# Performance work log

Hardware: AMD Instinct MI355X
Metric: run time of the kernel (lower is better)

Reference implementation:

```python
import jax, jax.numpy as jnp
import numpy as np

EMBED_DIM = 1024
NUM_HEADS = 16
HEAD_DIM = EMBED_DIM // NUM_HEADS
SEQ_LEN = 2048
B = 2


def setup_inputs() -> dict:
    key = jax.random.key(0)
    ks = jax.random.split(key, 6)
    x = jax.random.normal(ks[0], (B, SEQ_LEN, EMBED_DIM), dtype=jnp.float32)
    # Linear params (torch Linear: y = x @ W.T + b); store W as [in, out] for einsum
    qkv_w = jax.random.normal(ks[1], (EMBED_DIM, 3 * EMBED_DIM), dtype=jnp.float32) * (EMBED_DIM ** -0.5)
    qkv_b = jnp.zeros((3 * EMBED_DIM,), dtype=jnp.float32)
    proj_w = jax.random.normal(ks[2], (EMBED_DIM, EMBED_DIM), dtype=jnp.float32) * (EMBED_DIM ** -0.5)
    proj_b = jnp.zeros((EMBED_DIM,), dtype=jnp.float32)
    # relative position bias table [2L-1, H], trunc_normal std=0.02 ~ normal*0.02
    bias_table = jax.random.normal(ks[3], (2 * SEQ_LEN - 1, NUM_HEADS), dtype=jnp.float32) * 0.02
    return {"x": x, "qkv_w": qkv_w, "qkv_b": qkv_b, "proj_w": proj_w, "proj_b": proj_b, "bias_table": bias_table}


def _rel_pos_index(L):
    coords = jnp.arange(L)
    return (coords[None, :] - coords[:, None]) + (SEQ_LEN - 1)  # [L, L] int


def reference(x, qkv_w, qkv_b, proj_w, proj_b, bias_table):
    Bsz, L, C = x.shape
    scale = HEAD_DIM ** -0.5
    qkv = x @ qkv_w + qkv_b                               # [B, L, 3C]
    qkv = qkv.reshape(Bsz, L, 3, NUM_HEADS, HEAD_DIM)
    q = jnp.transpose(qkv[:, :, 0], (0, 2, 1, 3))          # [B, H, L, D]
    k = jnp.transpose(qkv[:, :, 1], (0, 2, 1, 3))
    v = jnp.transpose(qkv[:, :, 2], (0, 2, 1, 3))
    attn = jnp.einsum('bhqd,bhkd->bhqk', q, k) * scale     # [B, H, L, L]
    rel_bias = bias_table[_rel_pos_index(L)]               # [L, L, H]
    attn = attn + jnp.transpose(rel_bias, (2, 0, 1))[None]  # broadcast over batch
    attn = jax.nn.softmax(attn, axis=-1)
    out = jnp.einsum('bhqk,bhkd->bhqd', attn, v)           # [B, H, L, D]
    out = jnp.transpose(out, (0, 2, 1, 3)).reshape(Bsz, L, C)
    return out @ proj_w + proj_b
```

## Files before the change

### kernel.cpp

```cpp
#include <hip/hip_runtime.h>

typedef short bf16x4 __attribute__((ext_vector_type(4)));
typedef short bf16x8 __attribute__((ext_vector_type(8)));
typedef float f32x4 __attribute__((ext_vector_type(4)));
typedef float f32x16 __attribute__((ext_vector_type(16)));

__device__ __forceinline__ unsigned short f2bf(float f) {
  union { float f; unsigned int u; } v; v.f = f;
  unsigned int r = v.u + 0x7FFFu + ((v.u >> 16) & 1u);
  return (unsigned short)(r >> 16);
}

__device__ __forceinline__ float exp2_fast(float x) {
  float r;
  asm("v_exp_f32 %0, %1" : "=v"(r) : "v"(x));
  return r;
}

__device__ __forceinline__ unsigned int cvt_pk_bf16(float lo, float hi) {
  unsigned int r;
  asm("v_cvt_pk_bf16_f32 %0, %1, %2" : "=v"(r) : "v"(lo), "v"(hi));
  return r;
}

__device__ __forceinline__ void gld_lds16(const void* g, void* l) {
  __builtin_amdgcn_global_load_lds(
      (const __attribute__((address_space(1))) unsigned int*)g,
      (__attribute__((address_space(3))) unsigned int*)l, 16, 0, 0);
}


__global__ __launch_bounds__(256) void k_convert_x(const float4* __restrict__ in,
                                                   ushort4* __restrict__ out) {
  int id = blockIdx.x * 256 + threadIdx.x;
  float4 v = in[id];
  ushort4 o;
  o.x = f2bf(v.x); o.y = f2bf(v.y); o.z = f2bf(v.z); o.w = f2bf(v.w);
  out[id] = o;
}

__global__ __launch_bounds__(256) void k_transpose_bf16(const float* __restrict__ in,
                                                        unsigned short* __restrict__ out,
                                                        int R, int C) {
  __shared__ float tile[32][33];
  int tx = threadIdx.x, ty = threadIdx.y;
  int c0 = blockIdx.x * 32, r0 = blockIdx.y * 32;
#pragma unroll
  for (int i = 0; i < 32; i += 8) tile[ty + i][tx] = in[(size_t)(r0 + ty + i) * C + c0 + tx];
  __syncthreads();
#pragma unroll
  for (int i = 0; i < 32; i += 8) out[(size_t)(c0 + ty + i) * R + r0 + tx] = f2bf(tile[tx][ty + i]);
}

__global__ __launch_bounds__(256) void k_bias_cols(const float* __restrict__ bt,
                                                   float* __restrict__ bh) {
  int i = blockIdx.x * 256 + threadIdx.x;
  if (i < 4095 * 16) bh[(i & 15) * 4096 + (i >> 4)] = bt[i] * 1.44269504089f;
}

template <int EPI>
__global__ __launch_bounds__(256) void k_gemm(const unsigned short* __restrict__ A,
                                              const unsigned short* __restrict__ Bt,
                                              const float* __restrict__ bias,
                                              float* __restrict__ Cf,
                                              unsigned short* __restrict__ qb,
                                              unsigned short* __restrict__ kb,
                                              unsigned short* __restrict__ vtb) {
  __shared__ unsigned short Alds[128 * 64];
  __shared__ unsigned short Blds[128 * 64];
  const int t = threadIdx.x;
  const int l = t & 63, w = t >> 6;
  const int l15 = l & 15, l4 = l >> 4;
  const int wm = w >> 1, wn = w & 1;
  const int bm = blockIdx.y * 128, bn = blockIdx.x * 128;

  const int srow = t >> 3;
  const int scl = (t & 7) ^ (srow & 7);
  const unsigned short* ag = A + (size_t)(bm + srow) * 1024 + scl * 8;
  const unsigned short* bg = Bt + (size_t)(bn + srow) * 1024 + scl * 8;

  f32x4 acc[4][4];
#pragma unroll
  for (int i = 0; i < 4; ++i)
#pragma unroll
    for (int j = 0; j < 4; ++j) acc[i][j] = (f32x4){0.f, 0.f, 0.f, 0.f};

  for (int kt = 0; kt < 16; ++kt) {
#pragma unroll
    for (int q = 0; q < 4; ++q) {
      gld_lds16(ag + (size_t)q * 32 * 1024 + kt * 64, &Alds[(q * 256 + t) * 8]);
      gld_lds16(bg + (size_t)q * 32 * 1024 + kt * 64, &Blds[(q * 256 + t) * 8]);
    }
    __syncthreads();
#pragma unroll
    for (int kc = 0; kc < 2; ++kc) {
      bf16x8 af[4], bv[4];
#pragma unroll
      for (int i = 0; i < 4; ++i) {
        int ra = wm * 64 + i * 16 + l15;
        af[i] = *(const bf16x8*)&Alds[ra * 64 + (((kc * 4 + l4) ^ (l15 & 7))) * 8];
        int rb = wn * 64 + i * 16 + l15;
        bv[i] = *(const bf16x8*)&Blds[rb * 64 + (((kc * 4 + l4) ^ (l15 & 7))) * 8];
      }
#pragma unroll
      for (int i = 0; i < 4; ++i)
#pragma unroll
        for (int jn = 0; jn < 4; ++jn)
          acc[i][jn] = __builtin_amdgcn_mfma_f32_16x16x32_bf16(af[i], bv[jn], acc[i][jn], 0, 0, 0);
    }
    __syncthreads();
  }

#pragma unroll
  for (int i = 0; i < 4; ++i) {
#pragma unroll
    for (int jn = 0; jn < 4; ++jn) {
      int n = bn + wn * 64 + jn * 16 + l15;
      float bval = bias[n];
#pragma unroll
      for (int j = 0; j < 4; ++j) {
        int m = bm + wm * 64 + i * 16 + l4 * 4 + j;
        float v = acc[i][jn][j] + bval;
        if (EPI == 0) {
          Cf[(size_t)m * 1024 + n] = v;
        } else {
          int which = n >> 10, hh = (n >> 6) & 15, d = n & 63;
          int bb = m >> 11, pos = m & 2047;
          int bhh = bb * 16 + hh;
          if (which == 0)
            qb[((size_t)bhh * 2048 + pos) * 64 + d] = f2bf(v * 0.18033688f);
          else if (which == 1)
            kb[((size_t)bhh * 2048 + pos) * 64 + d] = f2bf(v);
          else
            vtb[((size_t)bhh * 64 + d) * 2048 + pos] = f2bf(v);
        }
      }
    }
  }
}

__global__ __launch_bounds__(256) void k_attn(const unsigned short* __restrict__ qbuf,
                                              const unsigned short* __restrict__ kbuf,
                                              const unsigned short* __restrict__ vtbuf,
                                              const float* __restrict__ biash,
                                              unsigned short* __restrict__ aout) {
  __shared__ __align__(16) unsigned short Klds[2][64 * 64];
  __shared__ __align__(16) unsigned short Vlds[2][64 * 64];
  __shared__ __align__(16) float blds[4 * 2308];

  const int t = threadIdx.x;
  const int w = t >> 6, l = t & 63;
  const int l31 = l & 31, hi = l >> 5;
  const int bh = blockIdx.y;
  const int h = bh & 15, b = bh >> 4;
  const int qbase = blockIdx.x * 128;
  const int wq = qbase + w * 32;

  bf16x8 qB[4];
  {
    const unsigned short* qrow = qbuf + ((size_t)bh * 2048 + wq + l31) * 64;
#pragma unroll
    for (int ds = 0; ds < 4; ++ds) qB[ds] = *(const bf16x8*)&qrow[ds * 16 + hi * 8];
  }

  f32x16 O[2];
#pragma unroll
  for (int i = 0; i < 16; ++i) { O[0][i] = 0.f; O[1][i] = 0.f; }
  float m_run = -3e38f, l_run = 0.f;

  const int c0r = t >> 3, c0c = t & 7;
  const unsigned short* kg = kbuf + ((size_t)bh * 2048 + c0r) * 64 + c0c * 8;
  const unsigned short* vg = vtbuf + ((size_t)bh * 64 + c0r) * 2048 + c0c * 8;
  const int wKV = c0r * 64 + ((c0c ^ (c0r & 7)) * 8);

  {
    bf16x8 k0 = *(const bf16x8*)(kg);
    bf16x8 k1 = *(const bf16x8*)(kg + 32 * 64);
    bf16x8 v0 = *(const bf16x8*)(vg);
    bf16x8 v1 = *(const bf16x8*)(vg + 32 * 2048);
    *(bf16x8*)&Klds[0][wKV] = k0;
    *(bf16x8*)&Klds[0][wKV + 2048] = k1;
    *(bf16x8*)&Vlds[0][wKV] = v0;
    *(bf16x8*)&Vlds[0][wKV + 2048] = v1;
    const float* win = biash + h * 4096 + (1920 - qbase);
    for (int j = t; j < 2308; j += 256) {
#pragma unroll
      for (int c = 0; c < 4; ++c) {
        float v = (j + c <= 2174) ? win[j + c] : 0.f;
        blds[c * 2308 + j] = v;
      }
    }
  }
  __syncthreads();

  const int cb = (127 - l31) & 3;
  const float* bbase = blds + (cb * 2308 + 127 - l31 - 32 * w + 4 * hi - cb);

  for (int kt = 0; kt < 32; ++kt) {
    const int cur = kt & 1;

    bf16x8 kst0, kst1, vst0, vst1;
    if (kt < 31) {
      const unsigned short* kga = kg + (size_t)(kt + 1) * 4096;
      const unsigned short* vga = vg + (kt + 1) * 64;
      kst0 = *(const bf16x8*)(kga);
      kst1 = *(const bf16x8*)(kga + 32 * 64);
      vst0 = *(const bf16x8*)(vga);
      vst1 = *(const bf16x8*)(vga + 32 * 2048);
    }
    const int kbase = kt * 64;

    f32x16 sacc[2];
#pragma unroll
    for (int i = 0; i < 16; ++i) { sacc[0][i] = 0.f; sacc[1][i] = 0.f; }
    __builtin_amdgcn_s_setprio(1);
#pragma unroll
    for (int kt2 = 0; kt2 < 2; ++kt2) {
      int row = kt2 * 32 + l31;
      int rsw = row & 7;
#pragma unroll
      for (int ds = 0; ds < 4; ++ds) {
        bf16x8 ka = *(const bf16x8*)&Klds[cur][row * 64 + (((2 * ds + hi) ^ rsw) * 8)];
        sacc[kt2] = __builtin_amdgcn_mfma_f32_32x32x16_bf16(ka, qB[ds], sacc[kt2], 0, 0, 0);
      }
    }
    __builtin_amdgcn_s_setprio(0);

#pragma unroll
    for (int kt2 = 0; kt2 < 2; ++kt2)
#pragma unroll
      for (int g = 0; g < 4; ++g) {
        f32x4 bq = *(const f32x4*)&bbase[kbase + 32 * kt2 + 8 * g];
#pragma unroll
        for (int r = 0; r < 4; ++r) sacc[kt2][4 * g + r] += bq[r];
      }

    float mx;
    {
      float q0 = fmaxf(fmaxf(sacc[0][0], sacc[0][1]), fmaxf(sacc[0][2], sacc[0][3]));
      float q1 = fmaxf(fmaxf(sacc[0][4], sacc[0][5]), fmaxf(sacc[0][6], sacc[0][7]));
      float q2 = fmaxf(fmaxf(sacc[0][8], sacc[0][9]), fmaxf(sacc[0][10], sacc[0][11]));
      float q3 = fmaxf(fmaxf(sacc[0][12], sacc[0][13]), fmaxf(sacc[0][14], sacc[0][15]));
      float q4 = fmaxf(fmaxf(sacc[1][0], sacc[1][1]), fmaxf(sacc[1][2], sacc[1][3]));
      float q5 = fmaxf(fmaxf(sacc[1][4], sacc[1][5]), fmaxf(sacc[1][6], sacc[1][7]));
      float q6 = fmaxf(fmaxf(sacc[1][8], sacc[1][9]), fmaxf(sacc[1][10], sacc[1][11]));
      float q7 = fmaxf(fmaxf(sacc[1][12], sacc[1][13]), fmaxf(sacc[1][14], sacc[1][15]));
      mx = fmaxf(fmaxf(fmaxf(q0, q1), fmaxf(q2, q3)), fmaxf(fmaxf(q4, q5), fmaxf(q6, q7)));
      mx = fmaxf(mx, __shfl_xor(mx, 32));
    }

    if (__any(mx > m_run + 8.f)) {
      float mnew = fmaxf(m_run, mx);
      float alpha = exp2_fast(m_run - mnew);
      m_run = mnew;
      l_run *= alpha;
#pragma unroll
      for (int g = 0; g < 4; ++g)
#pragma unroll
        for (int r = 0; r < 4; ++r) {
          float a_lo = __shfl(alpha, 8 * g + r);
          float a_hi = __shfl(alpha, 8 * g + r + 4);
          float aq = hi ? a_hi : a_lo;
          O[0][4 * g + r] *= aq;
          O[1][4 * g + r] *= aq;
        }
    }

#pragma unroll
    for (int kt2 = 0; kt2 < 2; ++kt2)
#pragma unroll
      for (int i = 0; i < 16; ++i) sacc[kt2][i] = exp2_fast(sacc[kt2][i] - m_run);
    {
      float s0 = (sacc[0][0] + sacc[0][1]) + (sacc[0][2] + sacc[0][3]);
      float s1 = (sacc[0][4] + sacc[0][5]) + (sacc[0][6] + sacc[0][7]);
      float s2 = (sacc[0][8] + sacc[0][9]) + (sacc[0][10] + sacc[0][11]);
      float s3 = (sacc[0][12] + sacc[0][13]) + (sacc[0][14] + sacc[0][15]);
      float s4 = (sacc[1][0] + sacc[1][1]) + (sacc[1][2] + sacc[1][3]);
      float s5 = (sacc[1][4] + sacc[1][5]) + (sacc[1][6] + sacc[1][7]);
      float s6 = (sacc[1][8] + sacc[1][9]) + (sacc[1][10] + sacc[1][11]);
      float s7 = (sacc[1][12] + sacc[1][13]) + (sacc[1][14] + sacc[1][15]);
      float rs = ((s0 + s1) + (s2 + s3)) + ((s4 + s5) + (s6 + s7));
      rs += __shfl_xor(rs, 32);
      l_run += rs;
    }

    bf16x8 pa[2][2];
#pragma unroll
    for (int kt2 = 0; kt2 < 2; ++kt2)
#pragma unroll
      for (int mm = 0; mm < 2; ++mm) {
        union { unsigned int u[4]; bf16x8 v; } pk;
        pk.u[0] = cvt_pk_bf16(sacc[kt2][8 * mm + 0], sacc[kt2][8 * mm + 1]);
        pk.u[1] = cvt_pk_bf16(sacc[kt2][8 * mm + 2], sacc[kt2][8 * mm + 3]);
        pk.u[2] = cvt_pk_bf16(sacc[kt2][8 * mm + 4], sacc[kt2][8 * mm + 5]);
        pk.u[3] = cvt_pk_bf16(sacc[kt2][8 * mm + 6], sacc[kt2][8 * mm + 7]);
        pa[kt2][mm] = pk.v;
      }

    __builtin_amdgcn_s_setprio(1);
#pragma unroll
    for (int dt = 0; dt < 2; ++dt) {
      int row = dt * 32 + l31;
      int rsw = row & 7;
#pragma unroll
      for (int kt2 = 0; kt2 < 2; ++kt2)
#pragma unroll
        for (int mm = 0; mm < 2; ++mm) {
          int cA = (4 * kt2 + 2 * mm) ^ rsw;
          int cB = (4 * kt2 + 2 * mm + 1) ^ rsw;
          bf16x4 vlo = *(const bf16x4*)&Vlds[cur][row * 64 + cA * 8 + 4 * hi];
          bf16x4 vhi = *(const bf16x4*)&Vlds[cur][row * 64 + cB * 8 + 4 * hi];
          bf16x8 vb = __builtin_shufflevector(vlo, vhi, 0, 1, 2, 3, 4, 5, 6, 7);
          O[dt] = __builtin_amdgcn_mfma_f32_32x32x16_bf16(pa[kt2][mm], vb, O[dt], 0, 0, 0);
        }
    }
    __builtin_amdgcn_s_setprio(0);

    if (kt < 31) {
      *(bf16x8*)&Klds[cur ^ 1][wKV] = kst0;
      *(bf16x8*)&Klds[cur ^ 1][wKV + 2048] = kst1;
      *(bf16x8*)&Vlds[cur ^ 1][wKV] = vst0;
      *(bf16x8*)&Vlds[cur ^ 1][wKV + 2048] = vst1;
    }
    __syncthreads();
  }

  {
    float linv = 1.f / l_run;
#pragma unroll
    for (int g = 0; g < 4; ++g)
#pragma unroll
      for (int r = 0; r < 4; ++r) {
        float v_lo = __shfl(linv, 8 * g + r);
        float v_hi = __shfl(linv, 8 * g + r + 4);
        float sc = hi ? v_hi : v_lo;
        int q = wq + 8 * g + r + 4 * hi;
        size_t base = ((size_t)b * 2048 + q) * 1024 + h * 64 + l31;
        aout[base] = f2bf(O[0][4 * g + r] * sc);
        aout[base + 32] = f2bf(O[1][4 * g + r] * sc);
      }
  }
}


extern "C" void kernel_launch(void* const* d_in, const int* in_sizes, int n_in,
                              void* d_out, int out_size, void* d_ws, size_t ws_size,
                              hipStream_t stream) {
  const float* x = (const float*)d_in[0];
  const float* qkv_w = (const float*)d_in[1];
  const float* qkv_b = (const float*)d_in[2];
  const float* proj_w = (const float*)d_in[3];
  const float* proj_b = (const float*)d_in[4];
  const float* bias_table = (const float*)d_in[5];
  float* out = (float*)d_out;

  char* ws = (char*)d_ws;
  unsigned short* xb = (unsigned short*)(ws);
  unsigned short* wqkv = (unsigned short*)(ws + (size_t)(8u << 20));
  unsigned short* wproj = (unsigned short*)(ws + (size_t)(14u << 20));
  unsigned short* qb = (unsigned short*)(ws + (size_t)(16u << 20));
  unsigned short* kb = (unsigned short*)(ws + (size_t)(24u << 20));
  unsigned short* vtb = (unsigned short*)(ws + (size_t)(32u << 20));
  float* biash = (float*)(ws + (size_t)(40u << 20));

  unsigned short* attn_out = xb;

  k_convert_x<<<dim3(4096), dim3(256), 0, stream>>>((const float4*)x, (ushort4*)xb);
  k_transpose_bf16<<<dim3(96, 32), dim3(32, 8), 0, stream>>>(qkv_w, wqkv, 1024, 3072);
  k_transpose_bf16<<<dim3(32, 32), dim3(32, 8), 0, stream>>>(proj_w, wproj, 1024, 1024);
  k_bias_cols<<<dim3(256), dim3(256), 0, stream>>>(bias_table, biash);

  k_gemm<1><<<dim3(24, 32), dim3(256), 0, stream>>>(xb, wqkv, qkv_b, nullptr, qb, kb, vtb);
  k_attn<<<dim3(16, 32), dim3(256), 0, stream>>>(qb, kb, vtb, biash, attn_out);
  k_gemm<0><<<dim3(8, 32), dim3(256), 0, stream>>>(attn_out, wproj, proj_b, out, nullptr, nullptr,
                                                   nullptr);
}
```

Measured before the change: 168.8 us.

## Software-pipeline attention QK^T ahead of softmax and swizzle workgroups for XCD locality

The attention loop is restructured so the QK^T MFMAs for the next KV tile are issued while the softmax and PV of the current tile run. S tiles alternate between two register sets, and V moves to a triple-buffered LDS ring with prefetch two tiles ahead. Both the GEMM and attention kernels also remap workgroup IDs so consecutive blocks on the same XCD share rows or heads, which should improve L2 reuse. The cost is higher register pressure from the extra score accumulators and prefetch registers, plus more LDS, which may lower occupancy.

```diff
diff --git a/kernel.cpp b/kernel.cpp
--- a/kernel.cpp
+++ b/kernel.cpp
@@ -72,7 +72,13 @@
   const int l = t & 63, w = t >> 6;
   const int l15 = l & 15, l4 = l >> 4;
   const int wm = w >> 1, wn = w & 1;
-  const int bm = blockIdx.y * 128, bn = blockIdx.x * 128;
+
+  constexpr int NX = EPI ? 24 : 8;
+  constexpr int NWG = EPI ? 768 : 256;
+  const int hwid = blockIdx.x + NX * blockIdx.y;
+  const int swz = (hwid & 7) * (NWG >> 3) + (hwid >> 3);
+  const int bn = (swz % NX) * 128;
+  const int bm = (swz / NX) * 128;
 
   const int srow = t >> 3;
   const int scl = (t & 7) ^ (srow & 7);
@@ -145,15 +151,19 @@
                                               const float* __restrict__ biash,
                                               unsigned short* __restrict__ aout) {
   __shared__ __align__(16) unsigned short Klds[2][64 * 64];
-  __shared__ __align__(16) unsigned short Vlds[2][64 * 64];
+  __shared__ __align__(16) unsigned short Vlds[3 * 64 * 64];
   __shared__ __align__(16) float blds[4 * 2308];
 
   const int t = threadIdx.x;
   const int w = t >> 6, l = t & 63;
   const int l31 = l & 31, hi = l >> 5;
-  const int bh = blockIdx.y;
+
+  const int bid = blockIdx.x;
+  const int swzb = (bid & 7) * 64 + (bid >> 3);
+  const int qt = swzb & 15;
+  const int bh = swzb >> 4;
   const int h = bh & 15, b = bh >> 4;
-  const int qbase = blockIdx.x * 128;
+  const int qbase = qt * 128;
   const int wq = qbase + w * 32;
 
   bf16x8 qB[4];
@@ -173,15 +183,28 @@
   const unsigned short* vg = vtbuf + ((size_t)bh * 64 + c0r) * 2048 + c0c * 8;
   const int wKV = c0r * 64 + ((c0c ^ (c0r & 7)) * 8);
 
+  bf16x8 kst0, kst1, vst0, vst1;
   {
-    bf16x8 k0 = *(const bf16x8*)(kg);
-    bf16x8 k1 = *(const bf16x8*)(kg + 32 * 64);
-    bf16x8 v0 = *(const bf16x8*)(vg);
-    bf16x8 v1 = *(const bf16x8*)(vg + 32 * 2048);
-    *(bf16x8*)&Klds[0][wKV] = k0;
-    *(bf16x8*)&Klds[0][wKV + 2048] = k1;
-    *(bf16x8*)&Vlds[0][wKV] = v0;
-    *(bf16x8*)&Vlds[0][wKV + 2048] = v1;
+    bf16x8 ka0 = *(const bf16x8*)(kg);
+    bf16x8 ka1 = *(const bf16x8*)(kg + 32 * 64);
+    bf16x8 va0 = *(const bf16x8*)(vg);
+    bf16x8 va1 = *(const bf16x8*)(vg + 32 * 2048);
+    bf16x8 kb0 = *(const bf16x8*)(kg + 4096);
+    bf16x8 kb1 = *(const bf16x8*)(kg + 4096 + 32 * 64);
+    bf16x8 vb0 = *(const bf16x8*)(vg + 64);
+    bf16x8 vb1 = *(const bf16x8*)(vg + 64 + 32 * 2048);
+    *(bf16x8*)&Klds[0][wKV] = ka0;
+    *(bf16x8*)&Klds[0][wKV + 2048] = ka1;
+    *(bf16x8*)&Vlds[wKV] = va0;
+    *(bf16x8*)&Vlds[wKV + 2048] = va1;
+    *(bf16x8*)&Klds[1][wKV] = kb0;
+    *(bf16x8*)&Klds[1][wKV + 2048] = kb1;
+    *(bf16x8*)&Vlds[4096 + wKV] = vb0;
+    *(bf16x8*)&Vlds[4096 + wKV + 2048] = vb1;
+    kst0 = *(const bf16x8*)(kg + 2 * 4096);
+    kst1 = *(const bf16x8*)(kg + 2 * 4096 + 32 * 64);
+    vst0 = *(const bf16x8*)(vg + 2 * 64);
+    vst1 = *(const bf16x8*)(vg + 2 * 64 + 32 * 2048);
     const float* win = biash + h * 4096 + (1920 - qbase);
     for (int j = t; j < 2308; j += 256) {
 #pragma unroll
@@ -196,134 +219,145 @@
   const int cb = (127 - l31) & 3;
   const float* bbase = blds + (cb * 2308 + 127 - l31 - 32 * w + 4 * hi - cb);
 
-  for (int kt = 0; kt < 32; ++kt) {
-    const int cur = kt & 1;
-
-    bf16x8 kst0, kst1, vst0, vst1;
-    if (kt < 31) {
-      const unsigned short* kga = kg + (size_t)(kt + 1) * 4096;
-      const unsigned short* vga = vg + (kt + 1) * 64;
-      kst0 = *(const bf16x8*)(kga);
-      kst1 = *(const bf16x8*)(kga + 32 * 64);
-      vst0 = *(const bf16x8*)(vga);
-      vst1 = *(const bf16x8*)(vga + 32 * 2048);
+  f32x16 sA[2], sB[2];
+
+#pragma unroll
+  for (int i = 0; i < 16; ++i) { sA[0][i] = 0.f; sA[1][i] = 0.f; }
+#pragma unroll
+  for (int kt2 = 0; kt2 < 2; ++kt2) {
+    int row = kt2 * 32 + l31;
+    int rsw = row & 7;
+#pragma unroll
+    for (int ds = 0; ds < 4; ++ds) {
+      bf16x8 ka = *(const bf16x8*)&Klds[0][row * 64 + (((2 * ds + hi) ^ rsw) * 8)];
+      sA[kt2] = __builtin_amdgcn_mfma_f32_32x32x16_bf16(ka, qB[ds], sA[kt2], 0, 0, 0);
     }
-    const int kbase = kt * 64;
-
-    f32x16 sacc[2];
-#pragma unroll
-    for (int i = 0; i < 16; ++i) { sacc[0][i] = 0.f; sacc[1][i] = 0.f; }
-    __builtin_amdgcn_s_setprio(1);
-#pragma unroll
-    for (int kt2 = 0; kt2 < 2; ++kt2) {
-      int row = kt2 * 32 + l31;
-      int rsw = row & 7;
-#pragma unroll
-      for (int ds = 0; ds < 4; ++ds) {
-        bf16x8 ka = *(const bf16x8*)&Klds[cur][row * 64 + (((2 * ds + hi) ^ rsw) * 8)];
-        sacc[kt2] = __builtin_amdgcn_mfma_f32_32x32x16_bf16(ka, qB[ds], sacc[kt2], 0, 0, 0);
-      }
-    }
-    __builtin_amdgcn_s_setprio(0);
-
-#pragma unroll
-    for (int kt2 = 0; kt2 < 2; ++kt2)
-#pragma unroll
-      for (int g = 0; g < 4; ++g) {
-        f32x4 bq = *(const f32x4*)&bbase[kbase + 32 * kt2 + 8 * g];
-#pragma unroll
-        for (int r = 0; r < 4; ++r) sacc[kt2][4 * g + r] += bq[r];
-      }
-
-    float mx;
-    {
-      float q0 = fmaxf(fmaxf(sacc[0][0], sacc[0][1]), fmaxf(sacc[0][2], sacc[0][3]));
-      float q1 = fmaxf(fmaxf(sacc[0][4], sacc[0][5]), fmaxf(sacc[0][6], sacc[0][7]));
-      float q2 = fmaxf(fmaxf(sacc[0][8], sacc[0][9]), fmaxf(sacc[0][10], sacc[0][11]));
-      float q3 = fmaxf(fmaxf(sacc[0][12], sacc[0][13]), fmaxf(sacc[0][14], sacc[0][15]));
-      float q4 = fmaxf(fmaxf(sacc[1][0], sacc[1][1]), fmaxf(sacc[1][2], sacc[1][3]));
-      float q5 = fmaxf(fmaxf(sacc[1][4], sacc[1][5]), fmaxf(sacc[1][6], sacc[1][7]));
-      float q6 = fmaxf(fmaxf(sacc[1][8], sacc[1][9]), fmaxf(sacc[1][10], sacc[1][11]));
-      float q7 = fmaxf(fmaxf(sacc[1][12], sacc[1][13]), fmaxf(sacc[1][14], sacc[1][15]));
-      mx = fmaxf(fmaxf(fmaxf(q0, q1), fmaxf(q2, q3)), fmaxf(fmaxf(q4, q5), fmaxf(q6, q7)));
-      mx = fmaxf(mx, __shfl_xor(mx, 32));
-    }
-
-    if (__any(mx > m_run + 8.f)) {
-      float mnew = fmaxf(m_run, mx);
-      float alpha = exp2_fast(m_run - mnew);
-      m_run = mnew;
-      l_run *= alpha;
-#pragma unroll
-      for (int g = 0; g < 4; ++g)
-#pragma unroll
-        for (int r = 0; r < 4; ++r) {
-          float a_lo = __shfl(alpha, 8 * g + r);
-          float a_hi = __shfl(alpha, 8 * g + r + 4);
-          float aq = hi ? a_hi : a_lo;
-          O[0][4 * g + r] *= aq;
-          O[1][4 * g + r] *= aq;
-        }
-    }
-
-#pragma unroll
-    for (int kt2 = 0; kt2 < 2; ++kt2)
-#pragma unroll
-      for (int i = 0; i < 16; ++i) sacc[kt2][i] = exp2_fast(sacc[kt2][i] - m_run);
-    {
-      float s0 = (sacc[0][0] + sacc[0][1]) + (sacc[0][2] + sacc[0][3]);
-      float s1 = (sacc[0][4] + sacc[0][5]) + (sacc[0][6] + sacc[0][7]);
-      float s2 = (sacc[0][8] + sacc[0][9]) + (sacc[0][10] + sacc[0][11]);
-      float s3 = (sacc[0][12] + sacc[0][13]) + (sacc[0][14] + sacc[0][15]);
-      float s4 = (sacc[1][0] + sacc[1][1]) + (sacc[1][2] + sacc[1][3]);
-      float s5 = (sacc[1][4] + sacc[1][5]) + (sacc[1][6] + sacc[1][7]);
-      float s6 = (sacc[1][8] + sacc[1][9]) + (sacc[1][10] + sacc[1][11]);
-      float s7 = (sacc[1][12] + sacc[1][13]) + (sacc[1][14] + sacc[1][15]);
-      float rs = ((s0 + s1) + (s2 + s3)) + ((s4 + s5) + (s6 + s7));
-      rs += __shfl_xor(rs, 32);
-      l_run += rs;
-    }
-
-    bf16x8 pa[2][2];
-#pragma unroll
-    for (int kt2 = 0; kt2 < 2; ++kt2)
-#pragma unroll
-      for (int mm = 0; mm < 2; ++mm) {
-        union { unsigned int u[4]; bf16x8 v; } pk;
-        pk.u[0] = cvt_pk_bf16(sacc[kt2][8 * mm + 0], sacc[kt2][8 * mm + 1]);
-        pk.u[1] = cvt_pk_bf16(sacc[kt2][8 * mm + 2], sacc[kt2][8 * mm + 3]);
-        pk.u[2] = cvt_pk_bf16(sacc[kt2][8 * mm + 4], sacc[kt2][8 * mm + 5]);
-        pk.u[3] = cvt_pk_bf16(sacc[kt2][8 * mm + 6], sacc[kt2][8 * mm + 7]);
-        pa[kt2][mm] = pk.v;
-      }
-
-    __builtin_amdgcn_s_setprio(1);
-#pragma unroll
-    for (int dt = 0; dt < 2; ++dt) {
-      int row = dt * 32 + l31;
-      int rsw = row & 7;
-#pragma unroll
-      for (int kt2 = 0; kt2 < 2; ++kt2)
-#pragma unroll
-        for (int mm = 0; mm < 2; ++mm) {
-          int cA = (4 * kt2 + 2 * mm) ^ rsw;
-          int cB = (4 * kt2 + 2 * mm + 1) ^ rsw;
-          bf16x4 vlo = *(const bf16x4*)&Vlds[cur][row * 64 + cA * 8 + 4 * hi];
-          bf16x4 vhi = *(const bf16x4*)&Vlds[cur][row * 64 + cB * 8 + 4 * hi];
-          bf16x8 vb = __builtin_shufflevector(vlo, vhi, 0, 1, 2, 3, 4, 5, 6, 7);
-          O[dt] = __builtin_amdgcn_mfma_f32_32x32x16_bf16(pa[kt2][mm], vb, O[dt], 0, 0, 0);
-        }
-    }
-    __builtin_amdgcn_s_setprio(0);
-
-    if (kt < 31) {
-      *(bf16x8*)&Klds[cur ^ 1][wKV] = kst0;
-      *(bf16x8*)&Klds[cur ^ 1][wKV + 2048] = kst1;
-      *(bf16x8*)&Vlds[cur ^ 1][wKV] = vst0;
-      *(bf16x8*)&Vlds[cur ^ 1][wKV + 2048] = vst1;
-    }
-    __syncthreads();
-  }
+  }
+  __syncthreads();
+
+  int vw_off = 2 * 4096;
+  int vr_off = 0;
+
+#define ATTN_PHASE(I, SCUR, SNXT, KW, KR)                                              \
+  {                                                                                    \
+    const int i_ = (I);                                                                \
+        \
+    if (i_ + 2 <= 31) {                                                                \
+      *(bf16x8*)&Klds[KW][wKV] = kst0;                                                 \
+      *(bf16x8*)&Klds[KW][wKV + 2048] = kst1;                                          \
+      *(bf16x8*)&Vlds[vw_off + wKV] = vst0;                                            \
+      *(bf16x8*)&Vlds[vw_off + wKV + 2048] = vst1;                                     \
+    }                                                                                  \
+                                                      \
+    if (i_ + 3 <= 31) {                                                                \
+      const unsigned short* kga = kg + (size_t)(i_ + 3) * 4096;                        \
+      const unsigned short* vga = vg + (i_ + 3) * 64;                                  \
+      kst0 = *(const bf16x8*)(kga);                                                    \
+      kst1 = *(const bf16x8*)(kga + 32 * 64);                                          \
+      vst0 = *(const bf16x8*)(vga);                                                    \
+      vst1 = *(const bf16x8*)(vga + 32 * 2048);                                        \
+    }                                                                                  \
+             \
+    if (i_ + 1 <= 31) {                                                                \
+      _Pragma("unroll") for (int z = 0; z < 16; ++z) { SNXT[0][z] = 0.f; SNXT[1][z] = 0.f; } \
+      _Pragma("unroll") for (int kt2 = 0; kt2 < 2; ++kt2) {                            \
+        int row = kt2 * 32 + l31;                                                      \
+        int rsw = row & 7;                                                             \
+        _Pragma("unroll") for (int ds = 0; ds < 4; ++ds) {                             \
+          bf16x8 ka = *(const bf16x8*)&Klds[KR][row * 64 + (((2 * ds + hi) ^ rsw) * 8)]; \
+          SNXT[kt2] = __builtin_amdgcn_mfma_f32_32x32x16_bf16(ka, qB[ds], SNXT[kt2], 0, 0, 0); \
+        }                                                                              \
+      }                                                                                \
+    }                                                                                  \
+                                                      \
+    {                                                                                  \
+      const int kbase = i_ * 64;                                                       \
+      _Pragma("unroll") for (int kt2 = 0; kt2 < 2; ++kt2)                              \
+        _Pragma("unroll") for (int g = 0; g < 4; ++g) {                                \
+          f32x4 bq = *(const f32x4*)&bbase[kbase + 32 * kt2 + 8 * g];                  \
+          _Pragma("unroll") for (int r = 0; r < 4; ++r) SCUR[kt2][4 * g + r] += bq[r]; \
+        }                                                                              \
+      float mx;                                                                        \
+      {                                                                                \
+        float q0 = fmaxf(fmaxf(SCUR[0][0], SCUR[0][1]), fmaxf(SCUR[0][2], SCUR[0][3]));\
+        float q1 = fmaxf(fmaxf(SCUR[0][4], SCUR[0][5]), fmaxf(SCUR[0][6], SCUR[0][7]));\
+        float q2 = fmaxf(fmaxf(SCUR[0][8], SCUR[0][9]), fmaxf(SCUR[0][10], SCUR[0][11]));\
+        float q3 = fmaxf(fmaxf(SCUR[0][12], SCUR[0][13]), fmaxf(SCUR[0][14], SCUR[0][15]));\
+        float q4 = fmaxf(fmaxf(SCUR[1][0], SCUR[1][1]), fmaxf(SCUR[1][2], SCUR[1][3]));\
+        float q5 = fmaxf(fmaxf(SCUR[1][4], SCUR[1][5]), fmaxf(SCUR[1][6], SCUR[1][7]));\
+        float q6 = fmaxf(fmaxf(SCUR[1][8], SCUR[1][9]), fmaxf(SCUR[1][10], SCUR[1][11]));\
+        float q7 = fmaxf(fmaxf(SCUR[1][12], SCUR[1][13]), fmaxf(SCUR[1][14], SCUR[1][15]));\
+        mx = fmaxf(fmaxf(fmaxf(q0, q1), fmaxf(q2, q3)), fmaxf(fmaxf(q4, q5), fmaxf(q6, q7)));\
+        mx = fmaxf(mx, __shfl_xor(mx, 32));                                            \
+      }                                                                                \
+      if (__any(mx > m_run + 8.f)) {                                                   \
+        float mnew = fmaxf(m_run, mx);                                                 \
+        float alpha = exp2_fast(m_run - mnew);                                         \
+        m_run = mnew;                                                                  \
+        l_run *= alpha;                                                                \
+        _Pragma("unroll") for (int g = 0; g < 4; ++g)                                  \
+          _Pragma("unroll") for (int r = 0; r < 4; ++r) {                              \
+            float a_lo = __shfl(alpha, 8 * g + r);                                     \
+            float a_hi = __shfl(alpha, 8 * g + r + 4);                                 \
+            float aq = hi ? a_hi : a_lo;                                               \
+            O[0][4 * g + r] *= aq;                                                     \
+            O[1][4 * g + r] *= aq;                                                     \
+          }                                                                            \
+      }                                                                                \
+      _Pragma("unroll") for (int kt2 = 0; kt2 < 2; ++kt2)                              \
+        _Pragma("unroll") for (int z = 0; z < 16; ++z)                                 \
+          SCUR[kt2][z] = exp2_fast(SCUR[kt2][z] - m_run);                              \
+      {                                                                                \
+        float s0 = (SCUR[0][0] + SCUR[0][1]) + (SCUR[0][2] + SCUR[0][3]);              \
+        float s1 = (SCUR[0][4] + SCUR[0][5]) + (SCUR[0][6] + SCUR[0][7]);              \
+        float s2 = (SCUR[0][8] + SCUR[0][9]) + (SCUR[0][10] + SCUR[0][11]);            \
+        float s3 = (SCUR[0][12] + SCUR[0][13]) + (SCUR[0][14] + SCUR[0][15]);          \
+        float s4 = (SCUR[1][0] + SCUR[1][1]) + (SCUR[1][2] + SCUR[1][3]);              \
+        float s5 = (SCUR[1][4] + SCUR[1][5]) + (SCUR[1][6] + SCUR[1][7]);              \
+        float s6 = (SCUR[1][8] + SCUR[1][9]) + (SCUR[1][10] + SCUR[1][11]);            \
+        float s7 = (SCUR[1][12] + SCUR[1][13]) + (SCUR[1][14] + SCUR[1][15]);          \
+        float rs = ((s0 + s1) + (s2 + s3)) + ((s4 + s5) + (s6 + s7));                  \
+        rs += __shfl_xor(rs, 32);                                                      \
+        l_run += rs;                                                                   \
+      }                                                                                \
+                                                                           \
+      bf16x8 pa[2][2];                                                                 \
+      _Pragma("unroll") for (int kt2 = 0; kt2 < 2; ++kt2)                              \
+        _Pragma("unroll") for (int mm = 0; mm < 2; ++mm) {                             \
+          union { unsigned int u[4]; bf16x8 v; } pk;                                   \
+          pk.u[0] = cvt_pk_bf16(SCUR[kt2][8 * mm + 0], SCUR[kt2][8 * mm + 1]);         \
+          pk.u[1] = cvt_pk_bf16(SCUR[kt2][8 * mm + 2], SCUR[kt2][8 * mm + 3]);         \
+          pk.u[2] = cvt_pk_bf16(SCUR[kt2][8 * mm + 4], SCUR[kt2][8 * mm + 5]);         \
+          pk.u[3] = cvt_pk_bf16(SCUR[kt2][8 * mm + 6], SCUR[kt2][8 * mm + 7]);         \
+          pa[kt2][mm] = pk.v;                                                          \
+        }                                                                              \
+                                                                         \
+      __builtin_amdgcn_s_setprio(1);                                                   \
+      _Pragma("unroll") for (int dt = 0; dt < 2; ++dt) {                               \
+        int row = dt * 32 + l31;                                                       \
+        int rsw = row & 7;                                                             \
+        _Pragma("unroll") for (int kt2 = 0; kt2 < 2; ++kt2)                            \
+          _Pragma("unroll") for (int mm = 0; mm < 2; ++mm) {                           \
+            int cA = (4 * kt2 + 2 * mm) ^ rsw;                                         \
+            int cB = (4 * kt2 + 2 * mm + 1) ^ rsw;                                     \
+            bf16x4 vlo = *(const bf16x4*)&Vlds[vr_off + row * 64 + cA * 8 + 4 * hi];   \
+            bf16x4 vhi = *(const bf16x4*)&Vlds[vr_off + row * 64 + cB * 8 + 4 * hi];   \
+            bf16x8 vb = __builtin_shufflevector(vlo, vhi, 0, 1, 2, 3, 4, 5, 6, 7);     \
+            O[dt] = __builtin_amdgcn_mfma_f32_32x32x16_bf16(pa[kt2][mm], vb, O[dt], 0, 0, 0); \
+          }                                                                            \
+      }                                                                                \
+      __builtin_amdgcn_s_setprio(0);                                                   \
+    }                                                                                  \
+    __syncthreads();                                                                   \
+    vw_off += 4096; if (vw_off == 3 * 4096) vw_off = 0;                                \
+    vr_off += 4096; if (vr_off == 3 * 4096) vr_off = 0;                                \
+  }
+
+  for (int i = 0; i < 32; i += 2) {
+    ATTN_PHASE(i, sA, sB, 0, 1);
+    ATTN_PHASE(i + 1, sB, sA, 1, 0);
+  }
+#undef ATTN_PHASE
 
   {
     float linv = 1.f / l_run;
@@ -371,7 +405,7 @@
   k_bias_cols<<<dim3(256), dim3(256), 0, stream>>>(bias_table, biash);
 
   k_gemm<1><<<dim3(24, 32), dim3(256), 0, stream>>>(xb, wqkv, qkv_b, nullptr, qb, kb, vtb);
-  k_attn<<<dim3(16, 32), dim3(256), 0, stream>>>(qb, kb, vtb, biash, attn_out);
+  k_attn<<<dim3(512), dim3(256), 0, stream>>>(qb, kb, vtb, biash, attn_out);
   k_gemm<0><<<dim3(8, 32), dim3(256), 0, stream>>>(attn_out, wproj, proj_b, out, nullptr, nullptr,
                                                    nullptr);
 }
```

Result: slower. 192.0 us (+13.7%).

## Swizzle workgroup IDs across XCDs and read relative bias directly from global

Applied to the files above, without the earlier changes.

Remaps the workgroup IDs of both GEMMs and the attention kernel so that consecutive IDs, which are dealt round-robin across the chiplets, land on tiles that share operands. This should raise L2 reuse of weight and K/V tiles. The attention kernel also drops the shared-memory copy of the bias window and loads unaligned f32x4 bias vectors straight from global memory each iteration. That frees LDS and removes a staging loop, at the cost of extra global and cache traffic and possible misaligned vector loads.

```diff
diff --git a/kernel.cpp b/kernel.cpp
--- a/kernel.cpp
+++ b/kernel.cpp
@@ -72,7 +72,13 @@
   const int l = t & 63, w = t >> 6;
   const int l15 = l & 15, l4 = l >> 4;
   const int wm = w >> 1, wn = w & 1;
-  const int bm = blockIdx.y * 128, bn = blockIdx.x * 128;
+
+  constexpr int NX = EPI ? 24 : 8;
+  constexpr int NWG = EPI ? 768 : 256;
+  const int hwid = blockIdx.x + NX * blockIdx.y;
+  const int swz = (hwid & 7) * (NWG >> 3) + (hwid >> 3);
+  const int bn = (swz % NX) * 128;
+  const int bm = (swz / NX) * 128;
 
   const int srow = t >> 3;
   const int scl = (t & 7) ^ (srow & 7);
@@ -146,14 +152,17 @@
                                               unsigned short* __restrict__ aout) {
   __shared__ __align__(16) unsigned short Klds[2][64 * 64];
   __shared__ __align__(16) unsigned short Vlds[2][64 * 64];
-  __shared__ __align__(16) float blds[4 * 2308];
 
   const int t = threadIdx.x;
   const int w = t >> 6, l = t & 63;
   const int l31 = l & 31, hi = l >> 5;
-  const int bh = blockIdx.y;
+
+  const int bid = blockIdx.x;
+  const int swzb = (bid & 7) * 64 + (bid >> 3);
+  const int qt = swzb & 15;
+  const int bh = swzb >> 4;
   const int h = bh & 15, b = bh >> 4;
-  const int qbase = blockIdx.x * 128;
+  const int qbase = qt * 128;
   const int wq = qbase + w * 32;
 
   bf16x8 qB[4];
@@ -182,19 +191,10 @@
     *(bf16x8*)&Klds[0][wKV + 2048] = k1;
     *(bf16x8*)&Vlds[0][wKV] = v0;
     *(bf16x8*)&Vlds[0][wKV + 2048] = v1;
-    const float* win = biash + h * 4096 + (1920 - qbase);
-    for (int j = t; j < 2308; j += 256) {
-#pragma unroll
-      for (int c = 0; c < 4; ++c) {
-        float v = (j + c <= 2174) ? win[j + c] : 0.f;
-        blds[c * 2308 + j] = v;
-      }
-    }
   }
   __syncthreads();
 
-  const int cb = (127 - l31) & 3;
-  const float* bbase = blds + (cb * 2308 + 127 - l31 - 32 * w + 4 * hi - cb);
+  const float* bgl = biash + h * 4096 + 2047 - (wq + l31) + 4 * hi;
 
   for (int kt = 0; kt < 32; ++kt) {
     const int cur = kt & 1;
@@ -210,6 +210,13 @@
     }
     const int kbase = kt * 64;
 
+    f32x4 bq[2][4];
+#pragma unroll
+    for (int kt2 = 0; kt2 < 2; ++kt2)
+#pragma unroll
+      for (int g = 0; g < 4; ++g)
+        __builtin_memcpy(&bq[kt2][g], &bgl[kbase + 32 * kt2 + 8 * g], 16);
+
     f32x16 sacc[2];
 #pragma unroll
     for (int i = 0; i < 16; ++i) { sacc[0][i] = 0.f; sacc[1][i] = 0.f; }
@@ -229,11 +236,9 @@
 #pragma unroll
     for (int kt2 = 0; kt2 < 2; ++kt2)
 #pragma unroll
-      for (int g = 0; g < 4; ++g) {
-        f32x4 bq = *(const f32x4*)&bbase[kbase + 32 * kt2 + 8 * g];
-#pragma unroll
-        for (int r = 0; r < 4; ++r) sacc[kt2][4 * g + r] += bq[r];
-      }
+      for (int g = 0; g < 4; ++g)
+#pragma unroll
+        for (int r = 0; r < 4; ++r) sacc[kt2][4 * g + r] += bq[kt2][g][r];
 
     float mx;
     {
@@ -371,7 +376,7 @@
   k_bias_cols<<<dim3(256), dim3(256), 0, stream>>>(bias_table, biash);
 
   k_gemm<1><<<dim3(24, 32), dim3(256), 0, stream>>>(xb, wqkv, qkv_b, nullptr, qb, kb, vtb);
-  k_attn<<<dim3(16, 32), dim3(256), 0, stream>>>(qb, kb, vtb, biash, attn_out);
+  k_attn<<<dim3(512), dim3(256), 0, stream>>>(qb, kb, vtb, biash, attn_out);
   k_gemm<0><<<dim3(8, 32), dim3(256), 0, stream>>>(attn_out, wproj, proj_b, out, nullptr, nullptr,
                                                    nullptr);
 }
```

New measurement: 161.9 us. 4.1% less time.
